# Optimization experiments

Measured on AMD Instinct MI355X. Metric: run time of the kernel, lower is better.

Reference implementation:

```python
import jax, jax.numpy as jnp
import numpy as np

C = 0.1            # args.hyp_c
EPS_PROJ = 4e-3    # hyptorch project eps for float32
MIN_NORM = 1e-5
NUM_HEADS = 12


def _norm(x):
    return jnp.maximum(jnp.linalg.norm(x, axis=-1, keepdims=True), MIN_NORM)


def expmap0(u, c):
    sqrt_c = c ** 0.5
    u_norm = _norm(u)
    return jnp.tanh(sqrt_c * u_norm) * u / (sqrt_c * u_norm)


def project(x, c):
    sqrt_c = c ** 0.5
    norm = _norm(x)
    maxnorm = (1.0 - EPS_PROJ) / sqrt_c
    return jnp.where(norm > maxnorm, x / norm * maxnorm, x)


def logmap0(y, c):
    sqrt_c = c ** 0.5
    y_norm = _norm(y)
    arg = jnp.clip(sqrt_c * y_norm, -1 + 1e-5, 1 - 1e-5)
    artanh = 0.5 * jnp.log((1 + arg) / (1 - arg))
    return y / (y_norm * sqrt_c) * artanh


def qkv_attention(x, wq, bq, wk, bk, wv, bv, num_heads):
    # x: [B, N, D]; weights in torch Linear convention [out, in]
    B, N, D = x.shape
    dh = D // num_heads
    q = (x @ wq.T + bq).reshape(B, N, num_heads, dh)
    k = (x @ wk.T + bk).reshape(B, N, num_heads, dh)
    v = (x @ wv.T + bv).reshape(B, N, num_heads, dh)
    # NOTE: original has no 1/sqrt(dh) scaling — keep faithful
    att = jnp.einsum('bnhd,bmhd->bhnm', q, k)
    att = jax.nn.softmax(att, axis=-1)
    out = jnp.einsum('bhnm,bmhd->bnhd', att, v)
    return out.reshape(B, N, D)


def setup_inputs() -> dict:
    key = jax.random.key(0)
    ks = jax.random.split(key, 7)
    B, N, D = 8, 1024, 768
    s = 0.02
    return {
        'x':   jax.random.normal(ks[0], (B, N, D), jnp.float32),
        'w_q': jax.random.normal(ks[1], (3, D, D), jnp.float32) * s,
        'b_q': jax.random.normal(ks[2], (3, D), jnp.float32) * s,
        'w_k': jax.random.normal(ks[3], (3, D, D), jnp.float32) * s,
        'b_k': jax.random.normal(ks[4], (3, D), jnp.float32) * s,
        'w_v': jax.random.normal(ks[5], (3, D, D), jnp.float32) * s,
        'b_v': jax.random.normal(ks[6], (3, D), jnp.float32) * s,
    }


def reference(x, w_q, b_q, w_k, b_k, w_v, b_v):
    # branch 0: euclidean; branch 1: hyperbolic (ToPoincare); branch 2: spherical (FromPoincare)
    x_e = x
    x_h = project(expmap0(x, C), C)
    x_s = logmap0(x, C)
    out = 0.0
    for i, xb in enumerate((x_e, x_h, x_s)):
        out = out + qkv_attention(xb, w_q[i], b_q[i], w_k[i], b_k[i],
                                  w_v[i], b_v[i], NUM_HEADS)
    return out
```

## Files before the change

kernel.cpp:

```cpp
#include <hip/hip_runtime.h>
#include <hip/hip_bf16.h>
#include <cstdint>
#include <cstddef>

#define B_   8
#define N_   1024
#define D_   768
#define H_   12
#define DH_  64
#define M_   (B_ * N_)
#define WSZ_ (D_ * D_)

typedef __bf16 bf16;
typedef bf16  bf16x8  __attribute__((ext_vector_type(8)));
typedef bf16  bf16x4  __attribute__((ext_vector_type(4)));
typedef float floatx4 __attribute__((ext_vector_type(4)));

#define MFMA16 __builtin_amdgcn_mfma_f32_16x16x32_bf16

__device__ __forceinline__ float exp2_fast(float x) {
    float r;
    asm("v_exp_f32 %0, %1" : "=v"(r) : "v"(x));
    return r;
}

__device__ __forceinline__ void gload_lds16(const void* g, void* l) {
    __builtin_amdgcn_global_load_lds(
        (const __attribute__((address_space(1))) unsigned int*)g,
        (__attribute__((address_space(3))) unsigned int*)l, 16, 0, 0);
}

__global__ __launch_bounds__(256) void prep_x(const float* __restrict__ x,
                                              bf16* __restrict__ xbf,
                                              float* __restrict__ sc ) {
    int row = blockIdx.x;
    int tid = threadIdx.x;
    const float* xr = x + (size_t)row * D_;
    bf16* xo = xbf + (size_t)row * D_;
    float v0 = xr[tid], v1 = xr[tid + 256], v2 = xr[tid + 512];
    xo[tid]       = (bf16)v0;
    xo[tid + 256] = (bf16)v1;
    xo[tid + 512] = (bf16)v2;
    float ss = v0 * v0 + v1 * v1 + v2 * v2;
    for (int off = 32; off; off >>= 1) ss += __shfl_xor(ss, off, 64);
    __shared__ float red[4];
    if ((tid & 63) == 0) red[tid >> 6] = ss;
    __syncthreads();
    if (tid == 0) {
        float t2 = red[0] + red[1] + red[2] + red[3];
        float t  = sqrtf(t2);
        const float scst = 0.31622776601683794f;
        float un = fmaxf(t, 1e-5f);
        float s1 = tanhf(scst * un) / (scst * un);
        float nh = fmaxf(t * s1, 1e-5f);
        float maxnorm = (1.0f - 4e-3f) / scst;
        float sh = (nh > maxnorm) ? s1 * (maxnorm / nh) : s1;
        float arg = fminf(scst * un, 1.0f - 1e-5f);
        float artanh = 0.5f * logf((1.0f + arg) / (1.0f - arg));
        float ssc = artanh / (un * scst);
        sc[row]      = sh;
        sc[M_ + row] = ssc;
    }
}

__global__ __launch_bounds__(256) void prep_w(const float* __restrict__ wq,
                                              const float* __restrict__ wk,
                                              const float* __restrict__ wv,
                                              bf16* __restrict__ wbf) {
    size_t i = ((size_t)blockIdx.x * 256 + threadIdx.x) * 4;
    int z = (int)(i / WSZ_);
    int r = (int)(i % WSZ_);
    int branch = z / 3, t = z % 3;
    const float* src = (t == 0 ? wq : t == 1 ? wk : wv) + (size_t)branch * WSZ_ + r;
    float4 f = *(const float4*)src;
    bf16x4 o = { (bf16)f.x, (bf16)f.y, (bf16)f.z, (bf16)f.w };
    *(bf16x4*)(wbf + i) = o;
}

#define NT9 12

#define STG(buf, mat, half, t) do {                                          \
    const bf16* _src = (mat) ? wbf : xbf;                                    \
    int _rb = ((mat) ? bn0 : bm0) + (half) * 128 + w * 16 + (lane >> 2);     \
    const bf16* _g = _src + (size_t)_rb * D_ + (t) * 64 + (lane & 3) * 8;    \
    bf16* _l = &L[buf][mat][half][0][w * 16][0];                             \
    gload_lds16(_g, _l);                                                     \
    gload_lds16(_g + 32, _l + 4096);                                         \
} while (0)

#define LOADA(buf, mh) do {                                                  \
    _Pragma("unroll") for (int fi = 0; fi < 4; fi++)                         \
    _Pragma("unroll") for (int kk = 0; kk < 2; kk++)                         \
        afr[fi][kk] = *(const bf16x8*)(&L[buf][0][wm][kk][(mh)*64 + fi*16 + c15][quad*8]); \
} while (0)

#define LOADB(buf, nh) do {                                                  \
    _Pragma("unroll") for (int fj = 0; fj < 2; fj++)                         \
    _Pragma("unroll") for (int kk = 0; kk < 2; kk++)                         \
        bfr[nh][fj][kk] = *(const bf16x8*)(&L[buf][1][wn>>1][kk][(wn&1)*64 + (nh)*32 + fj*16 + c15][quad*8]); \
} while (0)

#define MFMACL(mh, nh) do {                                                  \
    __builtin_amdgcn_s_setprio(1);                                           \
    _Pragma("unroll") for (int fi = 0; fi < 4; fi++)                         \
    _Pragma("unroll") for (int fj = 0; fj < 2; fj++)                         \
    _Pragma("unroll") for (int kk = 0; kk < 2; kk++)                         \
        acc[(mh)*4 + fi][(nh)*2 + fj] =                                      \
            MFMA16(afr[fi][kk], bfr[nh][fj][kk], acc[(mh)*4 + fi][(nh)*2 + fj], 0, 0, 0); \
    __builtin_amdgcn_s_setprio(0);                                           \
} while (0)

#define BAR() __builtin_amdgcn_s_barrier()
#define VMW4() asm volatile("s_waitcnt vmcnt(4)" ::: "memory")

__global__ __launch_bounds__(512, 2) void gemm_qkv9(
        const bf16* __restrict__ xbf, const bf16* __restrict__ wbf,
        const float* __restrict__ bq, const float* __restrict__ bk,
        const float* __restrict__ bv, const float* __restrict__ sc,
        bf16* __restrict__ qkv) {
    int bid = blockIdx.x;
    int v = (bid & 7) * 108 + (bid >> 3);
    int bx = v >> 5;
    int by = v & 31;
    int bn0 = bx * 256;
    int bm0 = by * 256;

    __shared__ bf16 L[2][2][2][2][128][32];

    int tid = threadIdx.x;
    int w = tid >> 6, lane = tid & 63;
    int wm = w >> 2, wn = w & 3;
    int quad = lane >> 4, c15 = lane & 15;

    bf16x8 afr[4][2];
    bf16x8 bfr[2][2][2];
    floatx4 acc[8][4];
#pragma unroll
    for (int i = 0; i < 8; i++)
#pragma unroll
        for (int j = 0; j < 4; j++) acc[i][j] = (floatx4){0.f, 0.f, 0.f, 0.f};

    STG(0, 0, 0, 0); STG(0, 0, 1, 0); STG(0, 1, 0, 0); STG(0, 1, 1, 0);
    STG(1, 1, 0, 1); STG(1, 1, 1, 1);
    VMW4();
    BAR();

    for (int it = 0; it < 6; it++) {
        int t1 = 2 * it + 1;
        bool st2 = (it < 5);
        LOADA(0, 0); LOADB(0, 0);
        STG(1, 0, 0, t1);
        BAR(); MFMACL(0, 0); BAR();
        LOADB(0, 1);
        STG(1, 0, 1, t1);
        BAR(); MFMACL(0, 1); BAR();
        LOADA(0, 1);
        if (st2) STG(0, 1, 0, t1 + 1);
        BAR(); MFMACL(1, 1); BAR();
        if (st2) STG(0, 1, 1, t1 + 1);
        VMW4();
        BAR(); MFMACL(1, 0); BAR();
        LOADA(1, 0); LOADB(1, 0);
        if (st2) STG(0, 0, 0, t1 + 1);
        BAR(); MFMACL(0, 0); BAR();
        LOADB(1, 1);
        if (st2) STG(0, 0, 1, t1 + 1);
        BAR(); MFMACL(0, 1); BAR();
        LOADA(1, 1);
        if (st2) STG(1, 1, 0, t1 + 2);
        BAR(); MFMACL(1, 1); BAR();
        if (st2) STG(1, 1, 1, t1 + 2);
        VMW4();
        BAR(); MFMACL(1, 0); BAR();
    }

    int gz = bn0 / 768;
    int branch = gz / 3, t = gz % 3;
    int colz0 = (bn0 % 768) + wn * 64;
    const float* bias = (t == 0 ? bq : t == 1 ? bk : bv) + branch * D_;
    const float* scb = (branch == 0) ? nullptr : sc + (size_t)(branch - 1) * M_;
    float bj[4];
#pragma unroll
    for (int fj = 0; fj < 4; fj++) bj[fj] = bias[colz0 + fj * 16 + c15];
    bf16* outz = qkv + (size_t)gz * M_ * D_;
#pragma unroll
    for (int fi = 0; fi < 8; fi++) {
        int rowbase = bm0 + wm * 128 + fi * 16 + quad * 4;
        float4 sv = scb ? *(const float4*)(scb + rowbase)
                        : (float4){1.f, 1.f, 1.f, 1.f};
        float svr[4] = { sv.x, sv.y, sv.z, sv.w };
#pragma unroll
        for (int r = 0; r < 4; r++) {
            bf16* orow = outz + (size_t)(rowbase + r) * D_;
#pragma unroll
            for (int fj = 0; fj < 4; fj++)
                orow[colz0 + fj * 16 + c15] = (bf16)(svr[r] * acc[fi][fj][r] + bj[fj]);
        }
    }
}

#define BM 128
#define BN 128
#define BK 32
__global__ __launch_bounds__(256) void gemm_qkv(
        const bf16* __restrict__ xbf, const bf16* __restrict__ wbf_all,
        const float* __restrict__ bq, const float* __restrict__ bk,
        const float* __restrict__ bv, const float* __restrict__ sc,
        int zoff, bf16* __restrict__ qkv) {
    int gz = zoff + blockIdx.z;
    int branch = gz / 3, t = gz % 3;
    const bf16*  wsrc = wbf_all + (size_t)gz * WSZ_;
    const float* bias = (t == 0 ? bq : t == 1 ? bk : bv) + branch * D_;
    bf16* out = qkv + (size_t)blockIdx.z * M_ * D_;
    int bm0 = blockIdx.y * BM;
    int bn0 = blockIdx.x * BN;

    __shared__ bf16 lA[BM * BK];
    __shared__ bf16 lB[BN * BK];

    int tid = threadIdx.x;
    int w = tid >> 6, lane = tid & 63;
    int wr = w >> 1, wc = w & 1;
    int quad = lane >> 4, c15 = lane & 15;
    int lrow = lane >> 2;
    int lcol = (lane & 3) * 8;

    floatx4 acc[4][4];
    for (int i = 0; i < 4; i++)
        for (int j = 0; j < 4; j++)
            acc[i][j] = (floatx4){0.f, 0.f, 0.f, 0.f};

    for (int k0 = 0; k0 < D_; k0 += BK) {
        const bf16* ga = xbf  + ((size_t)(bm0 + w * 32 + lrow) * D_ + k0 + lcol);
        const bf16* gb = wsrc + ((size_t)(bn0 + w * 32 + lrow) * D_ + k0 + lcol);
        gload_lds16(ga,           (char*)lA + w * 2048);
        gload_lds16(ga + 16 * D_, (char*)lA + w * 2048 + 1024);
        gload_lds16(gb,           (char*)lB + w * 2048);
        gload_lds16(gb + 16 * D_, (char*)lB + w * 2048 + 1024);
        __syncthreads();

        int arow = wr * 64 + c15;
        int brow = wc * 64 + c15;
        int kq = quad * 8;
        bf16x8 af[4], bfm[4];
        for (int i = 0; i < 4; i++) af[i]  = *(const bf16x8*)(lA + (arow + i * 16) * BK + kq);
        for (int j = 0; j < 4; j++) bfm[j] = *(const bf16x8*)(lB + (brow + j * 16) * BK + kq);
        for (int i = 0; i < 4; i++)
            for (int j = 0; j < 4; j++)
                acc[i][j] = MFMA16(af[i], bfm[j], acc[i][j], 0, 0, 0);
        __syncthreads();
    }

    const float* scb = (branch == 0) ? nullptr : sc + (size_t)(branch - 1) * M_;
    float bj[4];
    for (int j = 0; j < 4; j++) bj[j] = bias[bn0 + wc * 64 + j * 16 + c15];
    for (int i = 0; i < 4; i++) {
        int gRow0 = bm0 + wr * 64 + i * 16 + quad * 4;
        for (int r = 0; r < 4; r++) {
            float s = scb ? scb[gRow0 + r] : 1.0f;
            bf16* orow = out + (size_t)(gRow0 + r) * D_;
            for (int j = 0; j < 4; j++) {
                int gCol = bn0 + wc * 64 + j * 16 + c15;
                orow[gCol] = (bf16)(s * acc[i][j][r] + bj[j]);
            }
        }
    }
}

#define LDK 72
__global__ __launch_bounds__(256) void attn(const bf16* __restrict__ qkv,
                                            float* __restrict__ out) {
    int qt = blockIdx.x;
    int bh = blockIdx.y;
    int batch = bh / H_, head = bh % H_;
    int n0 = qt * 128;
    int tid = threadIdx.x, w = tid >> 6, lane = tid & 63;
    int quad = lane >> 4, c15 = lane & 15;

    const bf16* base = qkv + (size_t)blockIdx.z * 3 * M_ * D_;
    const bf16* qb = base;
    const bf16* kb = base + (size_t)M_ * D_;
    const bf16* vb = base + (size_t)2 * M_ * D_;
    size_t baseRow = (size_t)batch * N_;
    int colOff = head * DH_;

    __shared__ bf16 sK[64 * LDK];
    __shared__ bf16 sVt[64 * LDK];
    __shared__ bf16 sP[4][32 * LDK];
    bf16* sPw = sP[w];

    bf16x8 aq[2][2];
#pragma unroll
    for (int h = 0; h < 2; h++) {
        const bf16* qp = qb + ((baseRow + n0 + w * 32 + h * 16 + c15) * D_ + colOff + quad * 8);
        aq[h][0] = *(const bf16x8*)qp;
        aq[h][1] = *(const bf16x8*)(qp + 32);
#pragma unroll
        for (int f = 0; f < 2; f++)
#pragma unroll
            for (int i = 0; i < 8; i++)
                aq[h][f][i] = (bf16)((float)aq[h][f][i] * 1.4426950408889634f);
    }

    float m_sw[2] = { 0.f, 0.f };
    float l_sw[2] = { 0.f, 0.f };
    floatx4 o_acc[2][4];
#pragma unroll
    for (int h = 0; h < 2; h++)
#pragma unroll
        for (int j = 0; j < 4; j++) o_acc[h][j] = (floatx4){0.f, 0.f, 0.f, 0.f};

    int kkey = tid >> 3;
    int kcol = (tid & 7) << 3;
    int vkey = tid >> 2;
    int vd0  = (tid & 3) << 4;
    int vcol = vkey ^ ((tid & 3) << 4);

    const bf16* kg = kb + (baseRow + kkey) * D_ + colOff + kcol;
    const bf16* vg = vb + (baseRow + vkey) * D_ + colOff + vd0;

    bf16x8 kr0 = *(const bf16x8*)kg;
    bf16x8 kr1 = *(const bf16x8*)(kg + (size_t)32 * D_);
    bf16x8 vr0 = *(const bf16x8*)vg;
    bf16x8 vr1 = *(const bf16x8*)(vg + 8);

    for (int kt = 0; kt < 16; kt++) {
        if (kt) __syncthreads();
        *(bf16x8*)(sK + kkey * LDK + kcol)        = kr0;
        *(bf16x8*)(sK + (kkey + 32) * LDK + kcol) = kr1;
#pragma unroll
        for (int i = 0; i < 8; i++) sVt[(vd0 + i) * LDK + vcol]     = vr0[i];
#pragma unroll
        for (int i = 0; i < 8; i++) sVt[(vd0 + 8 + i) * LDK + vcol] = vr1[i];
        __syncthreads();
        if (kt < 15) {
            const bf16* kgn = kg + (size_t)(kt + 1) * 64 * D_;
            const bf16* vgn = vg + (size_t)(kt + 1) * 64 * D_;
            kr0 = *(const bf16x8*)kgn;
            kr1 = *(const bf16x8*)(kgn + (size_t)32 * D_);
            vr0 = *(const bf16x8*)vgn;
            vr1 = *(const bf16x8*)(vgn + 8);
        }

        floatx4 sfr[2][4];
        __builtin_amdgcn_s_setprio(1);
#pragma unroll
        for (int j = 0; j < 4; j++) {
            const bf16* kp = sK + (j * 16 + c15) * LDK + quad * 8;
            bf16x8 k0 = *(const bf16x8*)kp;
            bf16x8 k1 = *(const bf16x8*)(kp + 32);
#pragma unroll
            for (int h = 0; h < 2; h++) {
                floatx4 z = (floatx4){0.f, 0.f, 0.f, 0.f};
                z = MFMA16(k0, aq[h][0], z, 0, 0, 0);
                z = MFMA16(k1, aq[h][1], z, 0, 0, 0);
                sfr[h][j] = z;
            }
        }
        __builtin_amdgcn_s_setprio(0);

#pragma unroll
        for (int h = 0; h < 2; h++) {
            float mx = sfr[h][0][0];
#pragma unroll
            for (int j = 0; j < 4; j++)
#pragma unroll
                for (int r = 0; r < 4; r++) mx = fmaxf(mx, sfr[h][j][r]);
            if (__any(mx > m_sw[h] + 11.0f)) {
                float mr = fmaxf(mx, __shfl_xor(mx, 16, 64));
                mr = fmaxf(mr, __shfl_xor(mr, 32, 64));
                float mnew = fmaxf(m_sw[h], mr);
                float alpha = exp2_fast(m_sw[h] - mnew);
                l_sw[h] *= alpha;
                m_sw[h] = mnew;
#pragma unroll
                for (int r = 0; r < 4; r++) {
                    float a = __shfl(alpha, quad * 4 + r, 64);
#pragma unroll
                    for (int j = 0; j < 4; j++) o_acc[h][j][r] *= a;
                }
            }
            float m = m_sw[h];
            float sum = 0.f;
            bf16x4 pk[4];
#pragma unroll
            for (int j = 0; j < 4; j++)
#pragma unroll
                for (int r = 0; r < 4; r++) {
                    float p = exp2_fast(sfr[h][j][r] - m);
                    sum += p;
                    pk[j][r] = (bf16)p;
                }
            sum += __shfl_xor(sum, 16, 64);
            sum += __shfl_xor(sum, 32, 64);
            l_sw[h] += sum;
            bf16* pw = sPw + (h * 16 + c15) * LDK;
#pragma unroll
            for (int j = 0; j < 4; j++)
                *(bf16x4*)(pw + j * 16 + quad * 4) = pk[j];
        }

        asm volatile("s_waitcnt lgkmcnt(0)" ::: "memory");
        __builtin_amdgcn_sched_barrier(0);

        bf16x8 ap[2][2];
#pragma unroll
        for (int h = 0; h < 2; h++) {
            const bf16* pp = sPw + (h * 16 + c15) * LDK + quad * 8;
            ap[h][0] = *(const bf16x8*)pp;
            ap[h][1] = *(const bf16x8*)(pp + 32);
        }
        __builtin_amdgcn_s_setprio(1);
#pragma unroll
        for (int j = 0; j < 4; j++) {
            const bf16* vtp = sVt + (j * 16 + c15) * LDK;
            bf16x8 b0 = *(const bf16x8*)(vtp + ((quad * 8) ^ (16 * j)));
            bf16x8 b1 = *(const bf16x8*)(vtp + ((32 + quad * 8) ^ (16 * j)));
#pragma unroll
            for (int h = 0; h < 2; h++) {
                o_acc[h][j] = MFMA16(ap[h][0], b0, o_acc[h][j], 0, 0, 0);
                o_acc[h][j] = MFMA16(ap[h][1], b1, o_acc[h][j], 0, 0, 0);
            }
        }
        __builtin_amdgcn_s_setprio(0);
    }

#pragma unroll
    for (int h = 0; h < 2; h++) {
        float inv = 1.0f / l_sw[h];
#pragma unroll
        for (int r = 0; r < 4; r++) {
            float iv = __shfl(inv, quad * 4 + r, 64);
            int row = n0 + w * 32 + h * 16 + quad * 4 + r;
            float* op = out + ((size_t)batch * N_ + row) * D_ + colOff;
#pragma unroll
            for (int j = 0; j < 4; j++) {
                float v = o_acc[h][j][r] * iv;
                int col = j * 16 + c15;
                unsafeAtomicAdd(op + col, v);
            }
        }
    }
}

extern "C" void kernel_launch(void* const* d_in, const int* in_sizes, int n_in,
                              void* d_out, int out_size, void* d_ws, size_t ws_size,
                              hipStream_t stream) {
    const float* x  = (const float*)d_in[0];
    const float* wq = (const float*)d_in[1];
    const float* bq = (const float*)d_in[2];
    const float* wk = (const float*)d_in[3];
    const float* bk = (const float*)d_in[4];
    const float* wv = (const float*)d_in[5];
    const float* bv = (const float*)d_in[6];
    float* out = (float*)d_out;

    char* ws = (char*)d_ws;
    bf16*  xbf = (bf16*)ws;
    bf16*  wbf = (bf16*)(ws + 12582912);
    float* sc  = (float*)(ws + 12582912 + 10616832);
    bf16*  qkv = (bf16*)(ws + 12582912 + 10616832 + 65536);

    const size_t matB = (size_t)M_ * D_ * 2;
    const size_t need_all = 12582912 + 10616832 + 65536 + 9 * matB;

    hipMemsetAsync(d_out, 0, out_size, stream);
    hipLaunchKernelGGL(prep_x, dim3(M_), dim3(256), 0, stream, x, xbf, sc);
    hipLaunchKernelGGL(prep_w, dim3((9 * WSZ_ / 4) / 256), dim3(256), 0, stream, wq, wk, wv, wbf);

    if (ws_size >= need_all) {
        hipLaunchKernelGGL(gemm_qkv9, dim3(864), dim3(512), 0, stream,
                           xbf, wbf, bq, bk, bv, sc, qkv);
        hipLaunchKernelGGL(attn, dim3(N_ / 128, B_ * H_, 3), dim3(256), 0, stream,
                           qkv, out);
    } else {
        for (int br = 0; br < 3; br++) {
            hipLaunchKernelGGL(gemm_qkv, dim3(D_ / BN, M_ / BM, 3), dim3(256), 0, stream,
                               xbf, wbf, bq, bk, bv, sc, br * 3, qkv);
            hipLaunchKernelGGL(attn, dim3(N_ / 128, B_ * H_, 1), dim3(256), 0, stream,
                               qkv, out);
        }
    }
}
```

Baseline: 375.8 us.

## Write V pre-transposed from QKV GEMM and load V fragments directly in attention

```diff
diff --git a/kernel.cpp b/kernel.cpp
--- a/kernel.cpp
+++ b/kernel.cpp
@@ -189,12 +189,26 @@
         float4 sv = scb ? *(const float4*)(scb + rowbase)
                         : (float4){1.f, 1.f, 1.f, 1.f};
         float svr[4] = { sv.x, sv.y, sv.z, sv.w };
-#pragma unroll
-        for (int r = 0; r < 4; r++) {
-            bf16* orow = outz + (size_t)(rowbase + r) * D_;
-#pragma unroll
-            for (int fj = 0; fj < 4; fj++)
-                orow[colz0 + fj * 16 + c15] = (bf16)(svr[r] * acc[fi][fj][r] + bj[fj]);
+        if (t == 2) {
+            int b = rowbase >> 10, nn = rowbase & 1023;
+#pragma unroll
+            for (int fj = 0; fj < 4; fj++) {
+                int col = colz0 + fj * 16 + c15;
+                int h = col >> 6, dd = col & 63;
+                bf16x4 pkv;
+#pragma unroll
+                for (int r = 0; r < 4; r++)
+                    pkv[r] = (bf16)(svr[r] * acc[fi][fj][r] + bj[fj]);
+                *(bf16x4*)(outz + (((size_t)(b * H_ + h) * 64 + dd) << 10) + nn) = pkv;
+            }
+        } else {
+#pragma unroll
+            for (int r = 0; r < 4; r++) {
+                bf16* orow = outz + (size_t)(rowbase + r) * D_;
+#pragma unroll
+                for (int fj = 0; fj < 4; fj++)
+                    orow[colz0 + fj * 16 + c15] = (bf16)(svr[r] * acc[fi][fj][r] + bj[fj]);
+            }
         }
     }
 }
@@ -256,12 +270,25 @@
     for (int j = 0; j < 4; j++) bj[j] = bias[bn0 + wc * 64 + j * 16 + c15];
     for (int i = 0; i < 4; i++) {
         int gRow0 = bm0 + wr * 64 + i * 16 + quad * 4;
-        for (int r = 0; r < 4; r++) {
-            float s = scb ? scb[gRow0 + r] : 1.0f;
-            bf16* orow = out + (size_t)(gRow0 + r) * D_;
+        float s[4];
+        for (int r = 0; r < 4; r++) s[r] = scb ? scb[gRow0 + r] : 1.0f;
+        if (t == 2) {
+            int b = gRow0 >> 10, nn = gRow0 & 1023;
             for (int j = 0; j < 4; j++) {
-                int gCol = bn0 + wc * 64 + j * 16 + c15;
-                orow[gCol] = (bf16)(s * acc[i][j][r] + bj[j]);
+                int col = bn0 + wc * 64 + j * 16 + c15;
+                int h = col >> 6, dd = col & 63;
+                bf16x4 pkv;
+                for (int r = 0; r < 4; r++)
+                    pkv[r] = (bf16)(s[r] * acc[i][j][r] + bj[j]);
+                *(bf16x4*)(out + (((size_t)(b * H_ + h) * 64 + dd) << 10) + nn) = pkv;
+            }
+        } else {
+            for (int r = 0; r < 4; r++) {
+                bf16* orow = out + (size_t)(gRow0 + r) * D_;
+                for (int j = 0; j < 4; j++) {
+                    int gCol = bn0 + wc * 64 + j * 16 + c15;
+                    orow[gCol] = (bf16)(s[r] * acc[i][j][r] + bj[j]);
+                }
             }
         }
     }
@@ -272,20 +299,21 @@
                                             float* __restrict__ out) {
     int qt = blockIdx.x;
     int bh = blockIdx.y;
+    int br = blockIdx.z;
     int batch = bh / H_, head = bh % H_;
     int n0 = qt * 128;
     int tid = threadIdx.x, w = tid >> 6, lane = tid & 63;
     int quad = lane >> 4, c15 = lane & 15;
 
-    const bf16* base = qkv + (size_t)blockIdx.z * 3 * M_ * D_;
+    const bf16* base = qkv + (size_t)br * 3 * M_ * D_;
+    size_t baseRow = (size_t)batch * N_;
+    int colOff = head * DH_;
     const bf16* qb = base;
     const bf16* kb = base + (size_t)M_ * D_;
-    const bf16* vb = base + (size_t)2 * M_ * D_;
-    size_t baseRow = (size_t)batch * N_;
-    int colOff = head * DH_;
+    const bf16* vR = base + (size_t)2 * M_ * D_
+                   + ((size_t)(batch * H_ + head) * 64 + c15) * 1024 + quad * 8;
 
     __shared__ bf16 sK[64 * LDK];
-    __shared__ bf16 sVt[64 * LDK];
     __shared__ bf16 sP[4][32 * LDK];
     bf16* sPw = sP[w];
 
@@ -312,34 +340,27 @@
 
     int kkey = tid >> 3;
     int kcol = (tid & 7) << 3;
-    int vkey = tid >> 2;
-    int vd0  = (tid & 3) << 4;
-    int vcol = vkey ^ ((tid & 3) << 4);
-
     const bf16* kg = kb + (baseRow + kkey) * D_ + colOff + kcol;
-    const bf16* vg = vb + (baseRow + vkey) * D_ + colOff + vd0;
-
     bf16x8 kr0 = *(const bf16x8*)kg;
     bf16x8 kr1 = *(const bf16x8*)(kg + (size_t)32 * D_);
-    bf16x8 vr0 = *(const bf16x8*)vg;
-    bf16x8 vr1 = *(const bf16x8*)(vg + 8);
 
     for (int kt = 0; kt < 16; kt++) {
+        int m0 = kt * 64;
         if (kt) __syncthreads();
         *(bf16x8*)(sK + kkey * LDK + kcol)        = kr0;
         *(bf16x8*)(sK + (kkey + 32) * LDK + kcol) = kr1;
-#pragma unroll
-        for (int i = 0; i < 8; i++) sVt[(vd0 + i) * LDK + vcol]     = vr0[i];
-#pragma unroll
-        for (int i = 0; i < 8; i++) sVt[(vd0 + 8 + i) * LDK + vcol] = vr1[i];
         __syncthreads();
         if (kt < 15) {
             const bf16* kgn = kg + (size_t)(kt + 1) * 64 * D_;
-            const bf16* vgn = vg + (size_t)(kt + 1) * 64 * D_;
             kr0 = *(const bf16x8*)kgn;
             kr1 = *(const bf16x8*)(kgn + (size_t)32 * D_);
-            vr0 = *(const bf16x8*)vgn;
-            vr1 = *(const bf16x8*)(vgn + 8);
+        }
+        bf16x8 vf0[4], vf1[4];
+#pragma unroll
+        for (int j = 0; j < 4; j++) {
+            const bf16* vp = vR + (size_t)(j * 16) * 1024 + m0;
+            vf0[j] = *(const bf16x8*)vp;
+            vf1[j] = *(const bf16x8*)(vp + 32);
         }
 
         floatx4 sfr[2][4];
@@ -413,13 +434,10 @@
         __builtin_amdgcn_s_setprio(1);
 #pragma unroll
         for (int j = 0; j < 4; j++) {
-            const bf16* vtp = sVt + (j * 16 + c15) * LDK;
-            bf16x8 b0 = *(const bf16x8*)(vtp + ((quad * 8) ^ (16 * j)));
-            bf16x8 b1 = *(const bf16x8*)(vtp + ((32 + quad * 8) ^ (16 * j)));
 #pragma unroll
             for (int h = 0; h < 2; h++) {
-                o_acc[h][j] = MFMA16(ap[h][0], b0, o_acc[h][j], 0, 0, 0);
-                o_acc[h][j] = MFMA16(ap[h][1], b1, o_acc[h][j], 0, 0, 0);
+                o_acc[h][j] = MFMA16(ap[h][0], vf0[j], o_acc[h][j], 0, 0, 0);
+                o_acc[h][j] = MFMA16(ap[h][1], vf1[j], o_acc[h][j], 0, 0, 0);
             }
         }
         __builtin_amdgcn_s_setprio(0);
```

Measured after the change: 414.0 us. +10.2%, slower.
